# Performance work log

Hardware: AMD Instinct MI355X
Metric: run time of the kernel (lower is better)

The kernel has to match this reference:

```python
import jax, jax.numpy as jnp
from jax import lax
import numpy as np

B, T, IN, H, OUT = 8192, 512, 8, 64, 1


def setup_inputs() -> dict:
    key = jax.random.key(0)
    ks = jax.random.split(key, 7)
    s_ih = 1.0 / np.sqrt(H)
    # PyTorch LSTM param layout: gates stacked as [i, f, g, o] along dim 0
    W_ih = jax.random.uniform(ks[0], (4 * H, IN), jnp.float32, -s_ih, s_ih)
    W_hh = jax.random.uniform(ks[1], (4 * H, H), jnp.float32, -s_ih, s_ih)
    b_ih = jax.random.uniform(ks[2], (4 * H,), jnp.float32, -s_ih, s_ih)
    b_hh = jax.random.uniform(ks[3], (4 * H,), jnp.float32, -s_ih, s_ih)
    W_fc = jax.random.uniform(ks[4], (OUT, H), jnp.float32, -s_ih, s_ih)
    b_fc = jax.random.uniform(ks[5], (OUT,), jnp.float32, -s_ih, s_ih)
    x = jax.random.normal(ks[6], (B, T, IN), jnp.float32)
    return {"x": x, "W_ih": W_ih, "W_hh": W_hh, "b_ih": b_ih,
            "b_hh": b_hh, "W_fc": W_fc, "b_fc": b_fc}


def _lstm_last_h(x, W_ih, W_hh, b_ih, b_hh):
    # x: [B, T, IN] -> last hidden state [B, H]
    Bn = x.shape[0]
    Hn = W_hh.shape[1]
    b = b_ih + b_hh  # [4H]

    def step(carry, xt):
        h, c = carry  # [B, H] each
        gates = xt @ W_ih.T + h @ W_hh.T + b  # [B, 4H]
        i, f, g, o = jnp.split(gates, 4, axis=-1)
        i = jax.nn.sigmoid(i)
        f = jax.nn.sigmoid(f)
        g = jnp.tanh(g)
        o = jax.nn.sigmoid(o)
        c = f * c + i * g
        h = o * jnp.tanh(c)
        return (h, c), None

    h0 = jnp.zeros((Bn, Hn), x.dtype)
    c0 = jnp.zeros((Bn, Hn), x.dtype)
    (hT, _), _ = lax.scan(step, (h0, c0), jnp.swapaxes(x, 0, 1))  # scan over T
    return hT


def reference(x, W_ih, W_hh, b_ih, b_hh, W_fc, b_fc):
    hT = _lstm_last_h(x, W_ih, W_hh, b_ih, b_hh)  # [B, H]
    return hT @ W_fc.T + b_fc  # [B, OUT]
```

## Files before the change

### kernel.cpp

```cpp
#include <hip/hip_runtime.h>


typedef _Float16 f16_t;
typedef _Float16 half8 __attribute__((ext_vector_type(8)));
typedef __fp16 fp16x2 __attribute__((ext_vector_type(2)));
typedef float floatx4 __attribute__((ext_vector_type(4)));

#define Bn 8192
#define Tn 512
#define INn 8
#define Hn 64
#define BT 16
#define HSTRIDE 72

__global__ __launch_bounds__(256, 2)
void lstm_fused(const float* __restrict__ xg,
                const float* __restrict__ W_ih,
                const float* __restrict__ W_hh,
                const float* __restrict__ b_ih,
                const float* __restrict__ b_hh,
                const float* __restrict__ W_fc,
                const float* __restrict__ b_fc,
                float* __restrict__ out)
{
  __shared__ alignas(16) f16_t hbuf[2][BT][HSTRIDE];

  const int tid   = threadIdx.x;
  const int wv    = tid >> 6;
  const int lane  = tid & 63;
  const int n     = lane & 15;
  const int q     = lane >> 4;
  const int bbase = blockIdx.x * BT;

  const float LOG2E = 1.4426950408889634f;

  half8 bf[4][3];
  #pragma unroll
  for (int g = 0; g < 4; ++g) {
    const float sc = (g == 2) ? (2.f * LOG2E) : (-LOG2E);
    const int C = g * 64 + wv * 16 + n;
    #pragma unroll
    for (int c = 0; c < 3; ++c) {
      half8 v;
      #pragma unroll
      for (int j = 0; j < 8; ++j) {
        const int k = c * 32 + q * 8 + j;
        float w = 0.f;
        if (k < Hn)            w = W_hh[C * Hn + k] * sc;
        else if (k < Hn + INn) w = W_ih[C * INn + (k - Hn)] * sc;
        v[j] = (f16_t)w;
      }
      bf[g][c] = v;
    }
  }

  const int u = wv * 16 + n;
  const float pb_i = -(b_ih[u]       + b_hh[u])       * LOG2E;
  const float pb_f = -(b_ih[64 + u]  + b_hh[64 + u])  * LOG2E;
  const float pb_g =  (b_ih[128 + u] + b_hh[128 + u]) * (2.f * LOG2E);
  const float pb_o = -(b_ih[192 + u] + b_hh[192 + u]) * LOG2E;
  const floatx4 bi = {pb_i, pb_i, pb_i, pb_i};
  const floatx4 bfv = {pb_f, pb_f, pb_f, pb_f};
  const floatx4 bg = {pb_g, pb_g, pb_g, pb_g};
  const floatx4 bo = {pb_o, pb_o, pb_o, pb_o};

  for (int i = tid; i < BT * HSTRIDE; i += 256) ((f16_t*)hbuf[0])[i] = (f16_t)0.f;
  __syncthreads();

  const float* xp = xg + (size_t)(bbase + n) * Tn * INn;
  float4 xa = *(const float4*)(xp);
  float4 xb = *(const float4*)(xp + 4);

  float cst[4] = {0.f, 0.f, 0.f, 0.f};

  #pragma unroll 2
  for (int t = 0; t < Tn; ++t) {
    const int p  = t & 1;
    const int pn = p ^ 1;

    const half8 a0 = *(const half8*)&hbuf[p][n][q * 8];
    const half8 a1 = *(const half8*)&hbuf[p][n][32 + q * 8];

    union { half8 v; fp16x2 h2[4]; } A2;
    A2.h2[0] = __builtin_amdgcn_cvt_pkrtz(xa.x, xa.y);
    A2.h2[1] = __builtin_amdgcn_cvt_pkrtz(xa.z, xa.w);
    A2.h2[2] = __builtin_amdgcn_cvt_pkrtz(xb.x, xb.y);
    A2.h2[3] = __builtin_amdgcn_cvt_pkrtz(xb.z, xb.w);
    const half8 a2 = A2.v;

    const int tnx = (t + 1 < Tn) ? (t + 1) : 0;
    const float4 xan = *(const float4*)(xp + (size_t)tnx * INn);
    const float4 xbn = *(const float4*)(xp + (size_t)tnx * INn + 4);

    floatx4 ai = bi, af = bfv, ag = bg, ao = bo;
    ai = __builtin_amdgcn_mfma_f32_16x16x32_f16(a0, bf[0][0], ai, 0, 0, 0);
    ai = __builtin_amdgcn_mfma_f32_16x16x32_f16(a1, bf[0][1], ai, 0, 0, 0);
    ai = __builtin_amdgcn_mfma_f32_16x16x32_f16(a2, bf[0][2], ai, 0, 0, 0);
    af = __builtin_amdgcn_mfma_f32_16x16x32_f16(a0, bf[1][0], af, 0, 0, 0);
    af = __builtin_amdgcn_mfma_f32_16x16x32_f16(a1, bf[1][1], af, 0, 0, 0);
    af = __builtin_amdgcn_mfma_f32_16x16x32_f16(a2, bf[1][2], af, 0, 0, 0);
    ag = __builtin_amdgcn_mfma_f32_16x16x32_f16(a0, bf[2][0], ag, 0, 0, 0);
    ag = __builtin_amdgcn_mfma_f32_16x16x32_f16(a1, bf[2][1], ag, 0, 0, 0);
    ag = __builtin_amdgcn_mfma_f32_16x16x32_f16(a2, bf[2][2], ag, 0, 0, 0);
    ao = __builtin_amdgcn_mfma_f32_16x16x32_f16(a0, bf[3][0], ao, 0, 0, 0);
    ao = __builtin_amdgcn_mfma_f32_16x16x32_f16(a1, bf[3][1], ao, 0, 0, 0);
    ao = __builtin_amdgcn_mfma_f32_16x16x32_f16(a2, bf[3][2], ao, 0, 0, 0);

    float hv[4];
    #pragma unroll
    for (int r = 0; r < 4; ++r) {
      const float si = __builtin_amdgcn_rcpf(1.f + __builtin_amdgcn_exp2f(ai[r]));
      const float sf = __builtin_amdgcn_rcpf(1.f + __builtin_amdgcn_exp2f(af[r]));
      const float so = __builtin_amdgcn_rcpf(1.f + __builtin_amdgcn_exp2f(ao[r]));
      const float tg = __builtin_fmaf(
          -2.f, __builtin_amdgcn_rcpf(__builtin_amdgcn_exp2f(ag[r]) + 1.f), 1.f);
      const float cc = __builtin_fmaf(sf, cst[r], si * tg);
      cst[r] = cc;
      const float tc = __builtin_fmaf(
          -2.f,
          __builtin_amdgcn_rcpf(__builtin_amdgcn_exp2f(cc * (2.f * LOG2E)) + 1.f),
          1.f);
      hv[r] = so * tc;
    }
    #pragma unroll
    for (int r = 0; r < 4; ++r)
      hbuf[pn][q * 4 + r][u] = (f16_t)hv[r];

    xa = xan; xb = xbn;
    __syncthreads();
  }

  if (tid < 64) {
    const int b = lane & 15;
    const int part = lane >> 4;
    float s = 0.f;
    #pragma unroll
    for (int k = 0; k < 16; ++k) {
      const int uu = part * 16 + k;
      s = __builtin_fmaf((float)hbuf[0][b][uu], W_fc[uu], s);
    }
    s += __shfl_down(s, 32);
    s += __shfl_down(s, 16);
    if (lane < 16) out[bbase + b] = s + b_fc[0];
  }
}

extern "C" void kernel_launch(void* const* d_in, const int* in_sizes, int n_in,
                              void* d_out, int out_size, void* d_ws, size_t ws_size,
                              hipStream_t stream) {
  const float* x    = (const float*)d_in[0];
  const float* W_ih = (const float*)d_in[1];
  const float* W_hh = (const float*)d_in[2];
  const float* b_ih = (const float*)d_in[3];
  const float* b_hh = (const float*)d_in[4];
  const float* W_fc = (const float*)d_in[5];
  const float* b_fc = (const float*)d_in[6];
  float* out = (float*)d_out;
  dim3 grid(Bn / BT), block(256);
  hipLaunchKernelGGL(lstm_fused, grid, block, 0, stream,
                     x, W_ih, W_hh, b_ih, b_hh, W_fc, b_fc, out);
}
```

Measured before the change: 516.0 us.

## Stage input chunks of 16 timesteps in LDS via cooperative coalesced loads

Instead of each lane loading its own x row per timestep from global memory, the block cooperatively loads 16 timesteps for all 16 batch rows at once, converts them to fp16 and stores them in a double-buffered LDS tile. The next chunk is prefetched into registers while the current chunk is processed. This is meant to take per-step global load latency off the recurrence's critical path and make the loads more coalesced, at the cost of extra LDS and one extra barrier per chunk.

```diff
diff --git a/kernel.cpp b/kernel.cpp
--- a/kernel.cpp
+++ b/kernel.cpp
@@ -11,7 +11,10 @@
 #define INn 8
 #define Hn 64
 #define BT 16
+#define CHUNK 16
+#define NCHUNK (Tn / CHUNK)
 #define HSTRIDE 72
+#define XTSTRIDE 136
 
 __global__ __launch_bounds__(256, 2)
 void lstm_fused(const float* __restrict__ xg,
@@ -24,6 +27,7 @@
                 float* __restrict__ out)
 {
   __shared__ alignas(16) f16_t hbuf[2][BT][HSTRIDE];
+  __shared__ alignas(16) f16_t xlds[2][CHUNK][XTSTRIDE];
 
   const int tid   = threadIdx.x;
   const int wv    = tid >> 6;
@@ -65,69 +69,74 @@
   const floatx4 bo = {pb_o, pb_o, pb_o, pb_o};
 
   for (int i = tid; i < BT * HSTRIDE; i += 256) ((f16_t*)hbuf[0])[i] = (f16_t)0.f;
-  __syncthreads();
 
-  const float* xp = xg + (size_t)(bbase + n) * Tn * INn;
-  float4 xa = *(const float4*)(xp);
-  float4 xb = *(const float4*)(xp + 4);
+  const int row_s = tid >> 4;
+  const int tt_s  = tid & 15;
+  const float* xps = xg + ((size_t)(bbase + row_s) * Tn + tt_s) * INn;
+
+  float4 pa = *(const float4*)(xps);
+  float4 pb2 = *(const float4*)(xps + 4);
 
   float cst[4] = {0.f, 0.f, 0.f, 0.f};
 
-  #pragma unroll 2
-  for (int t = 0; t < Tn; ++t) {
-    const int p  = t & 1;
-    const int pn = p ^ 1;
+  for (int ch = 0; ch < NCHUNK; ++ch) {
+    union { half8 v; fp16x2 h2[4]; } P;
+    P.h2[0] = __builtin_amdgcn_cvt_pkrtz(pa.x, pa.y);
+    P.h2[1] = __builtin_amdgcn_cvt_pkrtz(pa.z, pa.w);
+    P.h2[2] = __builtin_amdgcn_cvt_pkrtz(pb2.x, pb2.y);
+    P.h2[3] = __builtin_amdgcn_cvt_pkrtz(pb2.z, pb2.w);
+    *(half8*)&xlds[ch & 1][tt_s][row_s * 8] = P.v;
+    __syncthreads();
 
-    const half8 a0 = *(const half8*)&hbuf[p][n][q * 8];
-    const half8 a1 = *(const half8*)&hbuf[p][n][32 + q * 8];
+    const int chn = (ch + 1 < NCHUNK) ? (ch + 1) : 0;
+    pa  = *(const float4*)(xps + (size_t)chn * CHUNK * INn);
+    pb2 = *(const float4*)(xps + (size_t)chn * CHUNK * INn + 4);
 
-    union { half8 v; fp16x2 h2[4]; } A2;
-    A2.h2[0] = __builtin_amdgcn_cvt_pkrtz(xa.x, xa.y);
-    A2.h2[1] = __builtin_amdgcn_cvt_pkrtz(xa.z, xa.w);
-    A2.h2[2] = __builtin_amdgcn_cvt_pkrtz(xb.x, xb.y);
-    A2.h2[3] = __builtin_amdgcn_cvt_pkrtz(xb.z, xb.w);
-    const half8 a2 = A2.v;
+    #pragma unroll
+    for (int tt = 0; tt < CHUNK; ++tt) {
+      const int p  = tt & 1;
+      const int pn = p ^ 1;
 
-    const int tnx = (t + 1 < Tn) ? (t + 1) : 0;
-    const float4 xan = *(const float4*)(xp + (size_t)tnx * INn);
-    const float4 xbn = *(const float4*)(xp + (size_t)tnx * INn + 4);
+      const half8 a0 = *(const half8*)&hbuf[p][n][q * 8];
+      const half8 a1 = *(const half8*)&hbuf[p][n][32 + q * 8];
+      const half8 a2 = *(const half8*)&xlds[ch & 1][tt][n * 8];
 
-    floatx4 ai = bi, af = bfv, ag = bg, ao = bo;
-    ai = __builtin_amdgcn_mfma_f32_16x16x32_f16(a0, bf[0][0], ai, 0, 0, 0);
-    ai = __builtin_amdgcn_mfma_f32_16x16x32_f16(a1, bf[0][1], ai, 0, 0, 0);
-    ai = __builtin_amdgcn_mfma_f32_16x16x32_f16(a2, bf[0][2], ai, 0, 0, 0);
-    af = __builtin_amdgcn_mfma_f32_16x16x32_f16(a0, bf[1][0], af, 0, 0, 0);
-    af = __builtin_amdgcn_mfma_f32_16x16x32_f16(a1, bf[1][1], af, 0, 0, 0);
-    af = __builtin_amdgcn_mfma_f32_16x16x32_f16(a2, bf[1][2], af, 0, 0, 0);
-    ag = __builtin_amdgcn_mfma_f32_16x16x32_f16(a0, bf[2][0], ag, 0, 0, 0);
-    ag = __builtin_amdgcn_mfma_f32_16x16x32_f16(a1, bf[2][1], ag, 0, 0, 0);
-    ag = __builtin_amdgcn_mfma_f32_16x16x32_f16(a2, bf[2][2], ag, 0, 0, 0);
-    ao = __builtin_amdgcn_mfma_f32_16x16x32_f16(a0, bf[3][0], ao, 0, 0, 0);
-    ao = __builtin_amdgcn_mfma_f32_16x16x32_f16(a1, bf[3][1], ao, 0, 0, 0);
-    ao = __builtin_amdgcn_mfma_f32_16x16x32_f16(a2, bf[3][2], ao, 0, 0, 0);
+      floatx4 ai = bi, af = bfv, ag = bg, ao = bo;
+      ai = __builtin_amdgcn_mfma_f32_16x16x32_f16(a0, bf[0][0], ai, 0, 0, 0);
+      ai = __builtin_amdgcn_mfma_f32_16x16x32_f16(a1, bf[0][1], ai, 0, 0, 0);
+      ai = __builtin_amdgcn_mfma_f32_16x16x32_f16(a2, bf[0][2], ai, 0, 0, 0);
+      af = __builtin_amdgcn_mfma_f32_16x16x32_f16(a0, bf[1][0], af, 0, 0, 0);
+      af = __builtin_amdgcn_mfma_f32_16x16x32_f16(a1, bf[1][1], af, 0, 0, 0);
+      af = __builtin_amdgcn_mfma_f32_16x16x32_f16(a2, bf[1][2], af, 0, 0, 0);
+      ag = __builtin_amdgcn_mfma_f32_16x16x32_f16(a0, bf[2][0], ag, 0, 0, 0);
+      ag = __builtin_amdgcn_mfma_f32_16x16x32_f16(a1, bf[2][1], ag, 0, 0, 0);
+      ag = __builtin_amdgcn_mfma_f32_16x16x32_f16(a2, bf[2][2], ag, 0, 0, 0);
+      ao = __builtin_amdgcn_mfma_f32_16x16x32_f16(a0, bf[3][0], ao, 0, 0, 0);
+      ao = __builtin_amdgcn_mfma_f32_16x16x32_f16(a1, bf[3][1], ao, 0, 0, 0);
+      ao = __builtin_amdgcn_mfma_f32_16x16x32_f16(a2, bf[3][2], ao, 0, 0, 0);
 
-    float hv[4];
-    #pragma unroll
-    for (int r = 0; r < 4; ++r) {
-      const float si = __builtin_amdgcn_rcpf(1.f + __builtin_amdgcn_exp2f(ai[r]));
-      const float sf = __builtin_amdgcn_rcpf(1.f + __builtin_amdgcn_exp2f(af[r]));
-      const float so = __builtin_amdgcn_rcpf(1.f + __builtin_amdgcn_exp2f(ao[r]));
-      const float tg = __builtin_fmaf(
-          -2.f, __builtin_amdgcn_rcpf(__builtin_amdgcn_exp2f(ag[r]) + 1.f), 1.f);
-      const float cc = __builtin_fmaf(sf, cst[r], si * tg);
-      cst[r] = cc;
-      const float tc = __builtin_fmaf(
-          -2.f,
-          __builtin_amdgcn_rcpf(__builtin_amdgcn_exp2f(cc * (2.f * LOG2E)) + 1.f),
-          1.f);
-      hv[r] = so * tc;
+      float hv[4];
+      #pragma unroll
+      for (int r = 0; r < 4; ++r) {
+        const float si = __builtin_amdgcn_rcpf(1.f + __builtin_amdgcn_exp2f(ai[r]));
+        const float sf = __builtin_amdgcn_rcpf(1.f + __builtin_amdgcn_exp2f(af[r]));
+        const float so = __builtin_amdgcn_rcpf(1.f + __builtin_amdgcn_exp2f(ao[r]));
+        const float tg = __builtin_fmaf(
+            -2.f, __builtin_amdgcn_rcpf(__builtin_amdgcn_exp2f(ag[r]) + 1.f), 1.f);
+        const float cc = __builtin_fmaf(sf, cst[r], si * tg);
+        cst[r] = cc;
+        const float tc = __builtin_fmaf(
+            -2.f,
+            __builtin_amdgcn_rcpf(__builtin_amdgcn_exp2f(cc * (2.f * LOG2E)) + 1.f),
+            1.f);
+        hv[r] = so * tc;
+      }
+      #pragma unroll
+      for (int r = 0; r < 4; ++r)
+        hbuf[pn][q * 4 + r][u] = (f16_t)hv[r];
+
+      __syncthreads();
     }
-    #pragma unroll
-    for (int r = 0; r < 4; ++r)
-      hbuf[pn][q * 4 + r][u] = (f16_t)hv[r];
-
-    xa = xan; xb = xbn;
-    __syncthreads();
   }
 
   if (tid < 64) {
```

New measurement: 496.3 us. 3.8% less time.
